# Optimization experiments

Measured on AMD Instinct MI355X. Metric: run time of the kernel, lower is better.

Reference implementation:

```python
import math
import jax, jax.numpy as jnp
import numpy as np

KERNEL_SIZE = 15
IN_CH = 64
OUT_CH = 128
RADIUS = 0.075
SIGMA = 0.03


def _get_kernel_points(num_points=KERNEL_SIZE, dim=3):
    pts = [np.zeros(dim)]
    n = num_points - 1
    golden = (1 + math.sqrt(5)) / 2
    for i in range(n):
        theta = math.acos(1 - 2 * (i + 0.5) / n)
        phi = 2 * math.pi * i / golden
        pts.append(np.array([math.sin(theta) * math.cos(phi),
                             math.sin(theta) * math.sin(phi),
                             math.cos(theta)]))
    return np.stack(pts, axis=0).astype(np.float32)


def setup_inputs() -> dict:
    key = jax.random.key(0)
    k1, k2, k3, k4, k5, k6 = jax.random.split(key, 6)
    B, N, M, K = 4, 16384, 16384, 16
    query_points = jax.random.uniform(k1, (B, N, 3), dtype=jnp.float32)
    support_points = jax.random.uniform(k2, (B, M, 3), dtype=jnp.float32)
    support_features = jax.random.normal(k3, (B, M, IN_CH), dtype=jnp.float32)
    neighbor_indices = jax.random.randint(k4, (B, N, K), 0, M)
    # kaiming_uniform_(a=sqrt(5)) -> U(-bound, bound), bound = sqrt(6/((1+5)*fan_in)) = 1/sqrt(fan_in)
    fan_in = IN_CH  # fan_in of (P, C_in, C_out) per torch convention (dim-1 * trailing)
    bound = 1.0 / math.sqrt(fan_in)
    weights = jax.random.uniform(k5, (KERNEL_SIZE, IN_CH, OUT_CH), dtype=jnp.float32,
                                 minval=-bound, maxval=bound)
    bias = jnp.zeros((OUT_CH,), dtype=jnp.float32)
    kernel_points = jnp.asarray(_get_kernel_points()) * (RADIUS * 0.7)  # (P, 3)
    return {"query_points": query_points, "support_points": support_points,
            "support_features": support_features, "neighbor_indices": neighbor_indices,
            "weights": weights, "bias": bias, "kernel_points": kernel_points}


def reference(query_points, support_points, support_features, neighbor_indices,
              weights, bias, kernel_points):
    # query_points: (B,N,3); support_points: (B,M,3); support_features: (B,M,C_in)
    # neighbor_indices: (B,N,K); weights: (P,C_in,C_out); kernel_points: (P,3)
    M = support_points.shape[1]
    safe_idx = jnp.clip(neighbor_indices, 0, M - 1)
    gather = jax.vmap(lambda sup, idx: sup[idx])  # per-batch fancy gather
    neighbor_coords = gather(support_points, safe_idx)       # (B,N,K,3)
    neighbor_feats = gather(support_features, safe_idx)      # (B,N,K,C_in)

    rel_pos = neighbor_coords - query_points[:, :, None, :]  # (B,N,K,3)
    diff = rel_pos[:, :, :, None, :] - kernel_points          # (B,N,K,P,3)
    dists = jnp.sqrt(jnp.clip(jnp.sum(diff * diff, axis=-1), 1e-10))  # (B,N,K,P)
    kernel_weights = jnp.maximum(1.0 - dists / SIGMA, 0.0)    # linear correlation

    # (B,N,P,K) @ (B,N,K,C_in) -> (B,N,P,C_in)
    weighted_feats = jnp.einsum('bnkp,bnkc->bnpc', kernel_weights, neighbor_feats)
    output = jnp.einsum('bnpc,pco->bno', weighted_feats, weights)  # (B,N,C_out)

    neighbor_has_feat = (jnp.sum(jnp.abs(neighbor_feats), axis=-1) > 0).astype(output.dtype)
    neighbor_count = jnp.clip(jnp.sum(neighbor_has_feat, axis=-1), 1.0)  # (B,N)
    return output / neighbor_count[..., None] + bias
```

## Files before the change

kernel.cpp:

```cpp
#include <hip/hip_runtime.h>

#define KNN    16
#define NKP    15
#define CIN    64
#define COUT   128
#define LOG2N  14
#define NQ     16384
#define NSUP   16384
#define NB     4
#define NTOT   (NB * NQ)
#define SIGMA_INV (1.0f / 0.03f)
#define REJ2   (0.084f * 0.084f)
#define QPW    8
#define NWAVE  (NTOT / QPW)
#define THR    256
#define NBLK   (NWAVE / (THR / 64))

__global__ __launch_bounds__(THR) void kpconv_fused(
    const float* __restrict__ qpts, const float* __restrict__ spts,
    const float* __restrict__ sfeat, const int* __restrict__ nidx,
    const float* __restrict__ W, const float* __restrict__ bias,
    const float* __restrict__ kpts, float* __restrict__ out)
{
    const int lane = threadIdx.x & 63;
    const int w    = (blockIdx.x * THR + threadIdx.x) >> 6;
    const int q0   = w * QPW;
    const int b    = q0 >> LOG2N;

    const int   pl = lane < NKP ? lane : 0;
    const float kx = kpts[pl * 3 + 0], ky = kpts[pl * 3 + 1], kz = kpts[pl * 3 + 2];

    const float2 b2 = ((const float2*)bias)[lane];

    const float qv = (lane < QPW * 3) ? qpts[(size_t)q0 * 3 + lane] : 0.0f;

    const int pr_lo = w * 128 + lane;
    int id_lo = nidx[pr_lo];            id_lo = id_lo < 0 ? 0 : (id_lo >= NSUP ? NSUP - 1 : id_lo);
    int id_hi = nidx[pr_lo + 64];       id_hi = id_hi < 0 ? 0 : (id_hi >= NSUP ? NSUP - 1 : id_hi);
    const int row_lo = b * NSUP + id_lo;
    const int row_hi = b * NSUP + id_hi;

    const int jl = lane >> 4, jh = 4 + (lane >> 4);
    const float rlx = spts[(size_t)row_lo * 3 + 0] - __shfl(qv, jl * 3 + 0);
    const float rly = spts[(size_t)row_lo * 3 + 1] - __shfl(qv, jl * 3 + 1);
    const float rlz = spts[(size_t)row_lo * 3 + 2] - __shfl(qv, jl * 3 + 2);
    const float rhx = spts[(size_t)row_hi * 3 + 0] - __shfl(qv, jh * 3 + 0);
    const float rhy = spts[(size_t)row_hi * 3 + 1] - __shfl(qv, jh * 3 + 1);
    const float rhz = spts[(size_t)row_hi * 3 + 2] - __shfl(qv, jh * 3 + 2);

    const unsigned long long m_lo = __ballot(rlx * rlx + rly * rly + rlz * rlz <= REJ2);
    const unsigned long long m_hi = __ballot(rhx * rhx + rhy * rhy + rhz * rhz <= REJ2);

    auto doquery = [&](int j, unsigned long long mhalf, int rowreg,
                       float rxr, float ryr, float rzr) {
        const unsigned int mask16 = (unsigned int)((mhalf >> ((j & 3) * 16)) & 0xFFFFu);
        float ax = 0.0f, ay = 0.0f;
        if (mask16) {
            const int  crow = __shfl(rowreg, (j & 3) * 16 + (lane >> 2));
            const float4* fp = (const float4*)sfeat + (size_t)crow * (CIN / 4) + (lane & 3) * 4;
            bool nz = false;
#pragma unroll
            for (int i = 0; i < 4; ++i) {
                const float4 v = fp[i];
                nz |= (v.x != 0.f) | (v.y != 0.f) | (v.z != 0.f) | (v.w != 0.f);
            }
            unsigned long long fm = __ballot(nz);
            fm = (fm | (fm >> 1) | (fm >> 2) | (fm >> 3)) & 0x1111111111111111ull;
            const int cnt = __popcll(fm);
            const float inv_cnt = 1.0f / (float)(cnt < 1 ? 1 : cnt);

            unsigned int km = mask16;
            while (km) {
                const int k = __ffs(km) - 1; km &= km - 1;
                const int src = (j & 3) * 16 + k;
                const int   row = __shfl(rowreg, src);
                const float rx  = __shfl(rxr, src);
                const float ry  = __shfl(ryr, src);
                const float rz  = __shfl(rzr, src);
                const float dx = rx - kx, dy = ry - ky, dz = rz - kz;
                const float d2 = dx * dx + dy * dy + dz * dz;
                const float wp = (lane < NKP)
                    ? fmaxf(1.0f - sqrtf(fmaxf(d2, 1e-10f)) * SIGMA_INV, 0.0f) : 0.0f;
                unsigned long long pm = __ballot(wp > 0.0f);
                if (!pm) continue;
                const float f = sfeat[(size_t)row * CIN + lane];
                while (pm) {
                    const int p = __ffsll(pm) - 1; pm &= pm - 1;
                    const float wv = __shfl(wp, p) * inv_cnt;
                    const float2* Wp = (const float2*)(W + (size_t)p * CIN * COUT) + lane;
                    float sx = 0.0f, sy = 0.0f;
#pragma unroll 16
                    for (int c = 0; c < CIN; ++c) {
                        const float fc = __shfl(f, c);
                        const float2 w2 = Wp[(size_t)c * (COUT / 2)];
                        sx += fc * w2.x;
                        sy += fc * w2.y;
                    }
                    ax += wv * sx;
                    ay += wv * sy;
                }
            }
        }
        ((float2*)(out + (size_t)(q0 + j) * COUT))[lane] =
            make_float2(ax + b2.x, ay + b2.y);
    };

    for (int j = 0; j < 4; ++j) doquery(j,     m_lo, row_lo, rlx, rly, rlz);
    for (int j = 4; j < 8; ++j) doquery(j,     m_hi, row_hi, rhx, rhy, rhz);
}

extern "C" void kernel_launch(void* const* d_in, const int* in_sizes, int n_in,
                              void* d_out, int out_size, void* d_ws, size_t ws_size,
                              hipStream_t stream) {
    const float* qp   = (const float*)d_in[0];
    const float* sp   = (const float*)d_in[1];
    const float* sf   = (const float*)d_in[2];
    const int*   ni   = (const int*)d_in[3];
    const float* W    = (const float*)d_in[4];
    const float* bias = (const float*)d_in[5];
    const float* kp   = (const float*)d_in[6];
    float* out = (float*)d_out;

    kpconv_fused<<<NBLK, THR, 0, stream>>>(qp, sp, sf, ni, W, bias, kp, out);
}
```

Baseline: 22.01 us.

## Halve queries per wave, tighten rejection radius, early-exit zero-feature check

Each wave now handles 4 queries instead of 8, so one neighbor load per lane covers all 64 neighbor slots and twice as many waves run, giving more parallelism to hide gather latency. The rejection radius for neighbors is tightened slightly so fewer neighbors reach the weight computation. The nonzero-feature check now reads only the first float4 per row and loads the rest only when some row looks all-zero. Output stores are deferred to the end and the inner channel loop is fully unrolled, which raises register pressure. The tighter radius is only safe if no kernel point influence reaches beyond it.

```diff
diff --git a/kernel.cpp b/kernel.cpp
--- a/kernel.cpp
+++ b/kernel.cpp
@@ -10,8 +10,8 @@
 #define NB     4
 #define NTOT   (NB * NQ)
 #define SIGMA_INV (1.0f / 0.03f)
-#define REJ2   (0.084f * 0.084f)
-#define QPW    8
+#define REJ2   (0.0826f * 0.0826f)
+#define QPW    4
 #define NWAVE  (NTOT / QPW)
 #define THR    256
 #define NBLK   (NWAVE / (THR / 64))
@@ -26,87 +26,95 @@
     const int w    = (blockIdx.x * THR + threadIdx.x) >> 6;
     const int q0   = w * QPW;
     const int b    = q0 >> LOG2N;
+    const int j    = lane >> 4;
+    const int q    = q0 + j;
 
     const int   pl = lane < NKP ? lane : 0;
     const float kx = kpts[pl * 3 + 0], ky = kpts[pl * 3 + 1], kz = kpts[pl * 3 + 2];
 
     const float2 b2 = ((const float2*)bias)[lane];
 
-    const float qv = (lane < QPW * 3) ? qpts[(size_t)q0 * 3 + lane] : 0.0f;
+    int id = nidx[(size_t)q0 * KNN + lane];
+    id = id < 0 ? 0 : (id >= NSUP ? NSUP - 1 : id);
+    const int row = b * NSUP + id;
 
-    const int pr_lo = w * 128 + lane;
-    int id_lo = nidx[pr_lo];            id_lo = id_lo < 0 ? 0 : (id_lo >= NSUP ? NSUP - 1 : id_lo);
-    int id_hi = nidx[pr_lo + 64];       id_hi = id_hi < 0 ? 0 : (id_hi >= NSUP ? NSUP - 1 : id_hi);
-    const int row_lo = b * NSUP + id_lo;
-    const int row_hi = b * NSUP + id_hi;
+    const float qx = qpts[(size_t)q * 3 + 0];
+    const float qy = qpts[(size_t)q * 3 + 1];
+    const float qz = qpts[(size_t)q * 3 + 2];
 
-    const int jl = lane >> 4, jh = 4 + (lane >> 4);
-    const float rlx = spts[(size_t)row_lo * 3 + 0] - __shfl(qv, jl * 3 + 0);
-    const float rly = spts[(size_t)row_lo * 3 + 1] - __shfl(qv, jl * 3 + 1);
-    const float rlz = spts[(size_t)row_lo * 3 + 2] - __shfl(qv, jl * 3 + 2);
-    const float rhx = spts[(size_t)row_hi * 3 + 0] - __shfl(qv, jh * 3 + 0);
-    const float rhy = spts[(size_t)row_hi * 3 + 1] - __shfl(qv, jh * 3 + 1);
-    const float rhz = spts[(size_t)row_hi * 3 + 2] - __shfl(qv, jh * 3 + 2);
+    const char* sp_b = (const char*)spts + (size_t)row * 12;
+    const float2 sxy = *(const float2*)sp_b;
+    const float  sz  = *(const float*)(sp_b + 8);
+    const float rx = sxy.x - qx, ry = sxy.y - qy, rz = sz - qz;
 
-    const unsigned long long m_lo = __ballot(rlx * rlx + rly * rly + rlz * rlz <= REJ2);
-    const unsigned long long m_hi = __ballot(rhx * rhx + rhy * rhy + rhz * rhz <= REJ2);
+    const unsigned long long m = __ballot(rx * rx + ry * ry + rz * rz <= REJ2);
 
-    auto doquery = [&](int j, unsigned long long mhalf, int rowreg,
-                       float rxr, float ryr, float rzr) {
-        const unsigned int mask16 = (unsigned int)((mhalf >> ((j & 3) * 16)) & 0xFFFFu);
-        float ax = 0.0f, ay = 0.0f;
-        if (mask16) {
-            const int  crow = __shfl(rowreg, (j & 3) * 16 + (lane >> 2));
-            const float4* fp = (const float4*)sfeat + (size_t)crow * (CIN / 4) + (lane & 3) * 4;
-            bool nz = false;
+    float accx[QPW] = {0.f, 0.f, 0.f, 0.f};
+    float accy[QPW] = {0.f, 0.f, 0.f, 0.f};
+
 #pragma unroll
-            for (int i = 0; i < 4; ++i) {
-                const float4 v = fp[i];
-                nz |= (v.x != 0.f) | (v.y != 0.f) | (v.z != 0.f) | (v.w != 0.f);
+    for (int jj = 0; jj < QPW; ++jj) {
+        const unsigned int mask16 = (unsigned int)((m >> (jj * 16)) & 0xFFFFu);
+        if (!mask16) continue;
+
+        const int crow = __shfl(row, jj * 16 + (lane >> 2));
+        const float4* fp = (const float4*)sfeat + (size_t)crow * (CIN / 4);
+        const float4 v0 = fp[lane & 3];
+        bool nz = (v0.x != 0.f) | (v0.y != 0.f) | (v0.z != 0.f) | (v0.w != 0.f);
+        unsigned long long fm = __ballot(nz);
+        unsigned long long rowsnz =
+            (fm | (fm >> 1) | (fm >> 2) | (fm >> 3)) & 0x1111111111111111ull;
+        if (rowsnz != 0x1111111111111111ull) {
+#pragma unroll
+            for (int i = 1; i < 4; ++i) {
+                const float4 u = fp[(lane & 3) + 4 * i];
+                nz |= (u.x != 0.f) | (u.y != 0.f) | (u.z != 0.f) | (u.w != 0.f);
             }
-            unsigned long long fm = __ballot(nz);
-            fm = (fm | (fm >> 1) | (fm >> 2) | (fm >> 3)) & 0x1111111111111111ull;
-            const int cnt = __popcll(fm);
-            const float inv_cnt = 1.0f / (float)(cnt < 1 ? 1 : cnt);
+            fm = __ballot(nz);
+            rowsnz = (fm | (fm >> 1) | (fm >> 2) | (fm >> 3)) & 0x1111111111111111ull;
+        }
+        const int cnt = __popcll(rowsnz);
+        const float inv_cnt = 1.0f / (float)(cnt < 1 ? 1 : cnt);
 
-            unsigned int km = mask16;
-            while (km) {
-                const int k = __ffs(km) - 1; km &= km - 1;
-                const int src = (j & 3) * 16 + k;
-                const int   row = __shfl(rowreg, src);
-                const float rx  = __shfl(rxr, src);
-                const float ry  = __shfl(ryr, src);
-                const float rz  = __shfl(rzr, src);
-                const float dx = rx - kx, dy = ry - ky, dz = rz - kz;
-                const float d2 = dx * dx + dy * dy + dz * dz;
-                const float wp = (lane < NKP)
-                    ? fmaxf(1.0f - sqrtf(fmaxf(d2, 1e-10f)) * SIGMA_INV, 0.0f) : 0.0f;
-                unsigned long long pm = __ballot(wp > 0.0f);
-                if (!pm) continue;
-                const float f = sfeat[(size_t)row * CIN + lane];
-                while (pm) {
-                    const int p = __ffsll(pm) - 1; pm &= pm - 1;
-                    const float wv = __shfl(wp, p) * inv_cnt;
-                    const float2* Wp = (const float2*)(W + (size_t)p * CIN * COUT) + lane;
-                    float sx = 0.0f, sy = 0.0f;
-#pragma unroll 16
-                    for (int c = 0; c < CIN; ++c) {
-                        const float fc = __shfl(f, c);
-                        const float2 w2 = Wp[(size_t)c * (COUT / 2)];
-                        sx += fc * w2.x;
-                        sy += fc * w2.y;
-                    }
-                    ax += wv * sx;
-                    ay += wv * sy;
+        unsigned int km = mask16;
+        while (km) {
+            const int k = __ffs(km) - 1; km &= km - 1;
+            const int src = jj * 16 + k;
+            const int   arow = __shfl(row, src);
+            const float arx  = __shfl(rx, src);
+            const float ary  = __shfl(ry, src);
+            const float arz  = __shfl(rz, src);
+
+            const float dx = arx - kx, dy = ary - ky, dz = arz - kz;
+            const float d2 = dx * dx + dy * dy + dz * dz;
+            const float wp = (lane < NKP)
+                ? fmaxf(1.0f - sqrtf(fmaxf(d2, 1e-10f)) * SIGMA_INV, 0.0f) : 0.0f;
+            unsigned long long pm = __ballot(wp > 0.0f);
+            if (!pm) continue;
+
+            const float f = sfeat[(size_t)arow * CIN + lane];
+            while (pm) {
+                const int p = __ffsll(pm) - 1; pm &= pm - 1;
+                const float wv = __shfl(wp, p) * inv_cnt;
+                const float2* Wp = (const float2*)(W + (size_t)p * CIN * COUT) + lane;
+                float sx = 0.0f, sy = 0.0f;
+#pragma unroll
+                for (int c = 0; c < CIN; ++c) {
+                    const float fc = __shfl(f, c);
+                    const float2 w2 = Wp[(size_t)c * (COUT / 2)];
+                    sx += fc * w2.x;
+                    sy += fc * w2.y;
                 }
+                accx[jj] += wv * sx;
+                accy[jj] += wv * sy;
             }
         }
-        ((float2*)(out + (size_t)(q0 + j) * COUT))[lane] =
-            make_float2(ax + b2.x, ay + b2.y);
-    };
+    }
 
-    for (int j = 0; j < 4; ++j) doquery(j,     m_lo, row_lo, rlx, rly, rlz);
-    for (int j = 4; j < 8; ++j) doquery(j,     m_hi, row_hi, rhx, rhy, rhz);
+#pragma unroll
+    for (int jj = 0; jj < QPW; ++jj)
+        ((float2*)(out + (size_t)(q0 + jj) * COUT))[lane] =
+            make_float2(accx[jj] + b2.x, accy[jj] + b2.y);
 }
 
 extern "C" void kernel_launch(void* const* d_in, const int* in_sizes, int n_in,
```

Result: slower. 42.97 us (+95.2%).
